# Performance work log

Measured on AMD Instinct MI355X. Metric: run time of the kernel, lower is better.

The kernel has to match this reference:

```python
import jax, jax.numpy as jnp
import numpy as np

TEMPERATURE = 0.04
LAMBDA_KOLEO = 0.1
EPS_NORM = 1e-12
EPS_KOLEO = 1e-9


def setup_inputs() -> dict:
    key = jax.random.key(0)
    k1, k2 = jax.random.split(key)
    N, D = 8192, 512
    z1 = jax.random.normal(k1, (N, D), dtype=jnp.float32)
    z2 = jax.random.normal(k2, (N, D), dtype=jnp.float32)
    return {"z1": z1, "z2": z2}


def _l2_normalize(x):
    # matches F.normalize(x, dim=1) with default eps=1e-12
    n = jnp.linalg.norm(x, axis=1, keepdims=True)
    return x / jnp.maximum(n, EPS_NORM)


def _infonce(queries, keys, temperature):
    # [N, N] similarity logits; labels are the diagonal
    logits = (queries @ keys.T) / temperature
    logp = jax.nn.log_softmax(logits, axis=1)
    return -jnp.mean(jnp.diagonal(logp))


def _koleo(emb):
    # pairwise euclidean distances via gram trick (matches torch.cdist p=2)
    sq = jnp.sum(emb * emb, axis=1)
    d2 = sq[:, None] + sq[None, :] - 2.0 * (emb @ emb.T)
    d = jnp.sqrt(jnp.maximum(d2, 0.0))
    N = emb.shape[0]
    eye = jnp.eye(N, dtype=bool)
    d = jnp.where(eye, jnp.inf, d)
    min_d = jnp.min(d, axis=1)
    return -jnp.mean(jnp.log(min_d + EPS_KOLEO))


def reference(z1, z2):
    z1 = _l2_normalize(z1)
    z2 = _l2_normalize(z2)
    loss_12 = _infonce(z1, z2, TEMPERATURE)
    loss_21 = _infonce(z2, z1, TEMPERATURE)
    loss_contrastive = (loss_12 + loss_21) / 2
    koleo_1 = _koleo(z1)
    koleo_2 = _koleo(z2)
    loss_koleo = (koleo_1 + koleo_2) / 2
    total_loss = loss_contrastive + LAMBDA_KOLEO * loss_koleo
    return total_loss
```

## Files before the change

kernel.cpp:

```cpp
#include <hip/hip_runtime.h>
#include <hip/hip_bf16.h>
#include <hip/hip_fp8.h>
#include <math.h>

#define N 8192
#define D 512
#define BM 128
#define BK 64
#define NSTRIP 64
#define S_BLOCKS (NSTRIP * NSTRIP)
#define TRI (NSTRIP * (NSTRIP + 1) / 2)
#define G_BLOCKS (2 * TRI)
#define SG_BLOCKS (S_BLOCKS + G_BLOCKS)

typedef float f32x16 __attribute__((ext_vector_type(16)));
typedef int i32x4 __attribute__((ext_vector_type(4)));
typedef int i32x8 __attribute__((ext_vector_type(8)));

__device__ inline void gload_lds16(const void* g, void* l) {
  __builtin_amdgcn_global_load_lds(
      (const __attribute__((address_space(1))) void*)g,
      (__attribute__((address_space(3))) void*)l, 16, 0, 0);
}

__global__ __launch_bounds__(256) void norm_kernel(
    const float* __restrict__ z1, const float* __restrict__ z2,
    unsigned char* __restrict__ q1, unsigned char* __restrict__ q2,
    float* __restrict__ diag, float* __restrict__ out) {
  int t = threadIdx.x;
  int lane = t & 63;
  int w = t >> 6;
  int row = blockIdx.x * 4 + w;
  if (blockIdx.x == 0 && t == 0) out[0] = 0.0f;
  const float4* a = (const float4*)(z1 + (size_t)row * D);
  const float4* b = (const float4*)(z2 + (size_t)row * D);
  float4 xa0 = a[lane], xa1 = a[lane + 64];
  float4 xb0 = b[lane], xb1 = b[lane + 64];
  float ss1 = xa0.x * xa0.x + xa0.y * xa0.y + xa0.z * xa0.z + xa0.w * xa0.w +
              xa1.x * xa1.x + xa1.y * xa1.y + xa1.z * xa1.z + xa1.w * xa1.w;
  float ss2 = xb0.x * xb0.x + xb0.y * xb0.y + xb0.z * xb0.z + xb0.w * xb0.w +
              xb1.x * xb1.x + xb1.y * xb1.y + xb1.z * xb1.z + xb1.w * xb1.w;
  float dd = xa0.x * xb0.x + xa0.y * xb0.y + xa0.z * xb0.z + xa0.w * xb0.w +
             xa1.x * xb1.x + xa1.y * xb1.y + xa1.z * xb1.z + xa1.w * xb1.w;
#pragma unroll
  for (int off = 1; off < 64; off <<= 1) {
    ss1 += __shfl_xor(ss1, off);
    ss2 += __shfl_xor(ss2, off);
    dd  += __shfl_xor(dd,  off);
  }
  float i1 = 1.0f / fmaxf(sqrtf(ss1), 1e-12f);
  float i2 = 1.0f / fmaxf(sqrtf(ss2), 1e-12f);
  float fa[8] = {xa0.x, xa0.y, xa0.z, xa0.w, xa1.x, xa1.y, xa1.z, xa1.w};
  float fb[8] = {xb0.x, xb0.y, xb0.z, xb0.w, xb1.x, xb1.y, xb1.z, xb1.w};
  unsigned int u1[2], u2[2];
#pragma unroll
  for (int g = 0; g < 2; g++) {
    unsigned int v1 = 0, v2 = 0;
#pragma unroll
    for (int e = 0; e < 4; e++) {
      __hip_fp8_e4m3 c1(fa[g * 4 + e] * i1);
      __hip_fp8_e4m3 c2(fb[g * 4 + e] * i2);
      v1 |= ((unsigned int)c1.__x) << (8 * e);
      v2 |= ((unsigned int)c2.__x) << (8 * e);
    }
    u1[g] = v1; u2[g] = v2;
  }
  ((unsigned int*)q1)[(size_t)row * 128 + lane] = u1[0];
  ((unsigned int*)q1)[(size_t)row * 128 + 64 + lane] = u1[1];
  ((unsigned int*)q2)[(size_t)row * 128 + lane] = u2[0];
  ((unsigned int*)q2)[(size_t)row * 128 + 64 + lane] = u2[1];
  if (lane == 0) diag[row] = dd * i1 * i2;
}

__device__ __forceinline__ void stage_chunk(
    const unsigned char* pA, const unsigned char* pB,
    unsigned char (*lds)[16384], int t, int chunk) {
  unsigned char* buf = lds[chunk & 1];
  int k0 = chunk * BK;
  gload_lds16(pA + k0,          buf + t * 16);
  gload_lds16(pA + 64 * D + k0, buf + 4096 + t * 16);
  gload_lds16(pB + k0,          buf + 8192 + t * 16);
  gload_lds16(pB + 64 * D + k0, buf + 12288 + t * 16);
}

#define SG_ROUND(p)                                                            \
  {                                                                            \
    asm volatile("s_waitcnt vmcnt(0)" ::: "memory");                           \
    __builtin_amdgcn_s_barrier();                                              \
    __builtin_amdgcn_sched_barrier(0);                                         \
    if ((p) < 7) stage_chunk(pA, pB, lds, t, (p) + 1);                         \
    const unsigned char* buf = lds[(p) & 1];                                   \
    i32x8 af[2], bf[2];                                                        \
    _Pragma("unroll")                                                          \
    for (int i = 0; i < 2; i++) {                                              \
      i32x4 lo = *(const i32x4*)(buf + offA[i]);                               \
      i32x4 hi = *(const i32x4*)(buf + (offA[i] ^ 16));                        \
      af[i] = __builtin_shufflevector(lo, hi, 0, 1, 2, 3, 4, 5, 6, 7);         \
      lo = *(const i32x4*)(buf + offB[i]);                                     \
      hi = *(const i32x4*)(buf + (offB[i] ^ 16));                              \
      bf[i] = __builtin_shufflevector(lo, hi, 0, 1, 2, 3, 4, 5, 6, 7);         \
    }                                                                          \
    asm volatile("s_waitcnt lgkmcnt(0)" ::: "memory");                         \
    __builtin_amdgcn_sched_barrier(0);                                         \
    __builtin_amdgcn_s_setprio(1);                                             \
    _Pragma("unroll")                                                          \
    for (int i = 0; i < 2; i++)                                                \
      _Pragma("unroll")                                                        \
      for (int j = 0; j < 2; j++)                                              \
        acc[i][j] = __builtin_amdgcn_mfma_scale_f32_32x32x64_f8f6f4(           \
            af[i], bf[j], acc[i][j], 0, 0, 0, 0x7F7F7F7F, 0, 0x7F7F7F7F);      \
    __builtin_amdgcn_s_setprio(0);                                             \
    __builtin_amdgcn_sched_barrier(0);                                         \
  }

__global__ __launch_bounds__(256, 4) void sg_kernel(
    const unsigned char* __restrict__ q1, const unsigned char* __restrict__ q2,
    float* __restrict__ rowS, float* __restrict__ colS,
    float* __restrict__ partG) {
  __shared__ unsigned char lds[2][16384];
  float (*redA)[BM] = reinterpret_cast<float (*)[BM]>(&lds[0][0]);
  float (*redB)[BM] = reinterpret_cast<float (*)[BM]>(&lds[0][0] + 1024);

  int bx = blockIdx.x;
  int t = threadIdx.x;
  int lane = t & 63;
  int wave = t >> 6;
  int l31 = lane & 31;
  int h = lane >> 5;
  int rw = wave >> 1;
  int cw = wave & 1;
  const float scale = 1.4426950408889634f / 0.04f;

  bool smode = bx < S_BLOCKS;
  const unsigned char* X;
  const unsigned char* Y;
  int r0, c0, ga = 0, gb = 0, gg = 0;
  bool diagb = false;
  if (smode) {
    r0 = (bx >> 6) * BM;
    c0 = (bx & 63) * BM;
    X = q1; Y = q2;
  } else {
    int gx = bx - S_BLOCKS;
    gg = (gx >= TRI) ? 1 : 0;
    int tri = gx - gg * TRI;
    int a = (int)((sqrtf(8.0f * (float)tri + 1.0f) - 1.0f) * 0.5f);
    while ((a + 1) * (a + 2) / 2 <= tri) a++;
    while (a * (a + 1) / 2 > tri) a--;
    int b = tri - a * (a + 1) / 2;
    ga = a; gb = b;
    X = gg ? q2 : q1; Y = X;
    r0 = a * BM;
    c0 = b * BM;
    diagb = (a == b);
  }

  int u = (l31 >> 4) & 1;
  int f = (l31 >> 1) & 3;
  int cs0 = (h << 1) ^ u ^ f;
  int offA[2], offB[2];
#pragma unroll
  for (int i = 0; i < 2; i++) {
    int rowa = rw * 64 + i * 32 + l31;
    offA[i] = rowa * 64 + cs0 * 16;
    int rowb = cw * 64 + i * 32 + l31;
    offB[i] = 8192 + rowb * 64 + cs0 * 16;
  }

  int srow = t >> 2;
  int ssrc = (t & 3) ^ ((t >> 3) & 3) ^ ((t >> 6) & 1);
  const unsigned char* pA = X + (size_t)(r0 + srow) * D + ssrc * 16;
  const unsigned char* pB = Y + (size_t)(c0 + srow) * D + ssrc * 16;

  f32x16 acc[2][2];
#pragma unroll
  for (int i = 0; i < 2; i++)
#pragma unroll
    for (int j = 0; j < 2; j++)
#pragma unroll
      for (int r = 0; r < 16; r++) acc[i][j][r] = 0.0f;

  stage_chunk(pA, pB, lds, t, 0);

  SG_ROUND(0) SG_ROUND(1) SG_ROUND(2) SG_ROUND(3)
  SG_ROUND(4) SG_ROUND(5) SG_ROUND(6) SG_ROUND(7)

  __syncthreads();

  if (smode) {
    float csum[2] = {0.0f, 0.0f};
#pragma unroll
    for (int i = 0; i < 2; i++) {
      float rsum[16];
#pragma unroll
      for (int reg = 0; reg < 16; reg++) rsum[reg] = 0.0f;
#pragma unroll
      for (int j = 0; j < 2; j++)
#pragma unroll
        for (int reg = 0; reg < 16; reg++) {
          float e = __builtin_amdgcn_exp2f(acc[i][j][reg] * scale);
          rsum[reg] += e;
          csum[j] += e;
        }
#pragma unroll
      for (int reg = 0; reg < 16; reg++) {
#pragma unroll
        for (int off = 1; off < 32; off <<= 1) rsum[reg] += __shfl_xor(rsum[reg], off);
      }
      if (l31 == 0) {
#pragma unroll
        for (int reg = 0; reg < 16; reg++) {
          int rloc = (reg & 3) + 8 * (reg >> 2) + 4 * h;
          redB[cw][rw * 64 + i * 32 + rloc] = rsum[reg];
        }
      }
    }
#pragma unroll
    for (int j = 0; j < 2; j++) {
      csum[j] += __shfl_xor(csum[j], 32);
      if (h == 0) redA[rw][cw * 64 + j * 32 + l31] = csum[j];
    }
    __syncthreads();
    if (t < BM) {
      colS[(size_t)(r0 >> 7) * N + c0 + t] = redA[0][t] + redA[1][t];
      rowS[(size_t)(c0 >> 7) * N + r0 + t] = redB[0][t] + redB[1][t];
    }
  } else {
#pragma unroll
    for (int i = 0; i < 2; i++) {
      float rmax[16];
#pragma unroll
      for (int reg = 0; reg < 16; reg++) {
        int rloc = (reg & 3) + 8 * (reg >> 2) + 4 * h;
        int rr = rw * 64 + i * 32 + rloc;
        float v = -3.0e38f;
#pragma unroll
        for (int j = 0; j < 2; j++) {
          float x = acc[i][j][reg];
          int cc = cw * 64 + j * 32 + l31;
          if (diagb && cc == rr) x = -3.0e38f;
          v = fmaxf(v, x);
        }
        rmax[reg] = v;
      }
#pragma unroll
      for (int reg = 0; reg < 16; reg++) {
#pragma unroll
        for (int off = 1; off < 32; off <<= 1) rmax[reg] = fmaxf(rmax[reg], __shfl_xor(rmax[reg], off));
      }
      if (l31 == 0) {
#pragma unroll
        for (int reg = 0; reg < 16; reg++) {
          int rloc = (reg & 3) + 8 * (reg >> 2) + 4 * h;
          redA[cw][rw * 64 + i * 32 + rloc] = rmax[reg];
        }
      }
    }
    if (!diagb) {
#pragma unroll
      for (int j = 0; j < 2; j++) {
        float m = -3.0e38f;
#pragma unroll
        for (int i = 0; i < 2; i++)
#pragma unroll
          for (int reg = 0; reg < 16; reg++) m = fmaxf(m, acc[i][j][reg]);
        m = fmaxf(m, __shfl_xor(m, 32));
        if (h == 0) redB[rw][cw * 64 + j * 32 + l31] = m;
      }
    }
    __syncthreads();
    if (t < BM) {
      partG[((size_t)(gg * NSTRIP + gb)) * N + r0 + t] = fmaxf(redA[0][t], redA[1][t]);
      if (!diagb)
        partG[((size_t)(gg * NSTRIP + ga)) * N + c0 + t] = fmaxf(redB[0][t], redB[1][t]);
    }
  }
}

__global__ __launch_bounds__(256) void combine_kernel(
    const float* __restrict__ diag,
    const float* __restrict__ rowS, const float* __restrict__ colS,
    const float* __restrict__ partG, float* __restrict__ out) {
  int t = threadIdx.x;
  int l = t & 63;
  int w = t >> 6;
  int i = blockIdx.x * 64 + l;

  float sR = 0.0f, sC = 0.0f, g1 = -3.0e38f, g2 = -3.0e38f;
#pragma unroll
  for (int s = 0; s < 16; s++) {
    int strip = w * 16 + s;
    sR += rowS[(size_t)strip * N + i];
    sC += colS[(size_t)strip * N + i];
    g1 = fmaxf(g1, partG[(size_t)strip * N + i]);
    g2 = fmaxf(g2, partG[(size_t)(NSTRIP + strip) * N + i]);
  }
  __shared__ float red[4][4][64];
  red[0][w][l] = sR; red[1][w][l] = sC; red[2][w][l] = g1; red[3][w][l] = g2;
  __syncthreads();
  if (w == 0) {
    sR = red[0][0][l] + red[0][1][l] + red[0][2][l] + red[0][3][l];
    sC = red[1][0][l] + red[1][1][l] + red[1][2][l] + red[1][3][l];
    g1 = fmaxf(fmaxf(red[2][0][l], red[2][1][l]), fmaxf(red[2][2][l], red[2][3][l]));
    g2 = fmaxf(fmaxf(red[3][0][l], red[3][1][l]), fmaxf(red[3][2][l], red[3][3][l]));
    float dv = diag[i] * 25.0f;
    float a12 = logf(sR) - dv;
    float a21 = logf(sC) - dv;
    float k1 = logf(sqrtf(fmaxf(2.0f - 2.0f * g1, 0.0f)) + 1e-9f);
    float k2 = logf(sqrtf(fmaxf(2.0f - 2.0f * g2, 0.0f)) + 1e-9f);
    float c = 0.5f * (a12 + a21) / (float)N - 0.1f * 0.5f * (k1 + k2) / (float)N;
#pragma unroll
    for (int off = 1; off < 64; off <<= 1) c += __shfl_xor(c, off);
    if (l == 0) atomicAdd(out, c);
  }
}

extern "C" void kernel_launch(void* const* d_in, const int* in_sizes, int n_in,
                              void* d_out, int out_size, void* d_ws, size_t ws_size,
                              hipStream_t stream) {
  const float* z1 = (const float*)d_in[0];
  const float* z2 = (const float*)d_in[1];
  char* w = (char*)d_ws;
  unsigned char* q1 = (unsigned char*)w; w += (size_t)N * D;
  unsigned char* q2 = (unsigned char*)w; w += (size_t)N * D;
  float* diag = (float*)w;   w += (size_t)N * sizeof(float);
  float* rowS = (float*)w;   w += (size_t)NSTRIP * N * sizeof(float);
  float* colS = (float*)w;   w += (size_t)NSTRIP * N * sizeof(float);
  float* partG = (float*)w;  w += (size_t)2 * NSTRIP * N * sizeof(float);
  float* out = (float*)d_out;

  norm_kernel<<<N / 4, 256, 0, stream>>>(z1, z2, q1, q2, diag, out);
  sg_kernel<<<SG_BLOCKS, 256, 0, stream>>>(q1, q2, rowS, colS, partG);
  combine_kernel<<<N / 64, 256, 0, stream>>>(diag, rowS, colS, partG, out);
}
```

Before: 199.9 us.

## Double K-chunk size to 128 with new LDS swizzle, halving barrier rounds

Raises the K staging chunk from 64 to 128 bytes, so each round loads a 128x128 fp8 tile of A and B into 32KB LDS buffers and issues two MFMA k-steps per round. The number of barrier and wait rounds drops from 8 to 4. LDS addressing changes to an XOR swizzle over 8 16-byte slots per 128-byte row. In exchange LDS use per block doubles and launch bounds drop from 4 to 2 blocks per CU, which lowers occupancy and the latency hiding it provides.

```diff
diff --git a/kernel.cpp b/kernel.cpp
--- a/kernel.cpp
+++ b/kernel.cpp
@@ -6,7 +6,7 @@
 #define N 8192
 #define D 512
 #define BM 128
-#define BK 64
+#define BK 128
 #define NSTRIP 64
 #define S_BLOCKS (NSTRIP * NSTRIP)
 #define TRI (NSTRIP * (NSTRIP + 1) / 2)
@@ -72,15 +72,15 @@
   if (lane == 0) diag[row] = dd * i1 * i2;
 }
 
-__device__ __forceinline__ void stage_chunk(
+__device__ __forceinline__ void stage_super(
     const unsigned char* pA, const unsigned char* pB,
-    unsigned char (*lds)[16384], int t, int chunk) {
-  unsigned char* buf = lds[chunk & 1];
-  int k0 = chunk * BK;
-  gload_lds16(pA + k0,          buf + t * 16);
-  gload_lds16(pA + 64 * D + k0, buf + 4096 + t * 16);
-  gload_lds16(pB + k0,          buf + 8192 + t * 16);
-  gload_lds16(pB + 64 * D + k0, buf + 12288 + t * 16);
+    unsigned char* buf, int t, int sc) {
+  int k0 = sc * BK;
+#pragma unroll
+  for (int it = 0; it < 4; it++) {
+    gload_lds16(pA + (size_t)(it * 32) * D + k0, buf + it * 4096 + t * 16);
+    gload_lds16(pB + (size_t)(it * 32) * D + k0, buf + 16384 + it * 4096 + t * 16);
+  }
 }
 
 #define SG_ROUND(p)                                                            \
@@ -88,36 +88,41 @@
     asm volatile("s_waitcnt vmcnt(0)" ::: "memory");                           \
     __builtin_amdgcn_s_barrier();                                              \
     __builtin_amdgcn_sched_barrier(0);                                         \
-    if ((p) < 7) stage_chunk(pA, pB, lds, t, (p) + 1);                         \
+    if ((p) < 3) stage_super(pA, pB, lds[((p) + 1) & 1], t, (p) + 1);          \
     const unsigned char* buf = lds[(p) & 1];                                   \
-    i32x8 af[2], bf[2];                                                        \
+    i32x8 af[2][2], bf[2][2];                                                  \
     _Pragma("unroll")                                                          \
-    for (int i = 0; i < 2; i++) {                                              \
-      i32x4 lo = *(const i32x4*)(buf + offA[i]);                               \
-      i32x4 hi = *(const i32x4*)(buf + (offA[i] ^ 16));                        \
-      af[i] = __builtin_shufflevector(lo, hi, 0, 1, 2, 3, 4, 5, 6, 7);         \
-      lo = *(const i32x4*)(buf + offB[i]);                                     \
-      hi = *(const i32x4*)(buf + (offB[i] ^ 16));                              \
-      bf[i] = __builtin_shufflevector(lo, hi, 0, 1, 2, 3, 4, 5, 6, 7);         \
-    }                                                                          \
+    for (int ks = 0; ks < 2; ks++)                                             \
+      _Pragma("unroll")                                                        \
+      for (int i = 0; i < 2; i++) {                                            \
+        i32x4 lo = *(const i32x4*)(buf + offA[ks][i]);                         \
+        i32x4 hi = *(const i32x4*)(buf + (offA[ks][i] ^ 16));                  \
+        af[ks][i] = __builtin_shufflevector(lo, hi, 0, 1, 2, 3, 4, 5, 6, 7);   \
+        lo = *(const i32x4*)(buf + offB[ks][i]);                               \
+        hi = *(const i32x4*)(buf + (offB[ks][i] ^ 16));                        \
+        bf[ks][i] = __builtin_shufflevector(lo, hi, 0, 1, 2, 3, 4, 5, 6, 7);   \
+      }                                                                        \
     asm volatile("s_waitcnt lgkmcnt(0)" ::: "memory");                         \
     __builtin_amdgcn_sched_barrier(0);                                         \
     __builtin_amdgcn_s_setprio(1);                                             \
     _Pragma("unroll")                                                          \
-    for (int i = 0; i < 2; i++)                                                \
+    for (int ks = 0; ks < 2; ks++)                                             \
       _Pragma("unroll")                                                        \
-      for (int j = 0; j < 2; j++)                                              \
-        acc[i][j] = __builtin_amdgcn_mfma_scale_f32_32x32x64_f8f6f4(           \
-            af[i], bf[j], acc[i][j], 0, 0, 0, 0x7F7F7F7F, 0, 0x7F7F7F7F);      \
+      for (int i = 0; i < 2; i++)                                              \
+        _Pragma("unroll")                                                      \
+        for (int j = 0; j < 2; j++)                                            \
+          acc[i][j] = __builtin_amdgcn_mfma_scale_f32_32x32x64_f8f6f4(         \
+              af[ks][i], bf[ks][j], acc[i][j], 0, 0, 0, 0x7F7F7F7F, 0,         \
+              0x7F7F7F7F);                                                     \
     __builtin_amdgcn_s_setprio(0);                                             \
     __builtin_amdgcn_sched_barrier(0);                                         \
   }
 
-__global__ __launch_bounds__(256, 4) void sg_kernel(
+__global__ __launch_bounds__(256, 2) void sg_kernel(
     const unsigned char* __restrict__ q1, const unsigned char* __restrict__ q2,
     float* __restrict__ rowS, float* __restrict__ colS,
     float* __restrict__ partG) {
-  __shared__ unsigned char lds[2][16384];
+  __shared__ unsigned char lds[2][32768];
   float (*redA)[BM] = reinterpret_cast<float (*)[BM]>(&lds[0][0]);
   float (*redB)[BM] = reinterpret_cast<float (*)[BM]>(&lds[0][0] + 1024);
 
@@ -155,20 +160,20 @@
     diagb = (a == b);
   }
 
-  int u = (l31 >> 4) & 1;
-  int f = (l31 >> 1) & 3;
-  int cs0 = (h << 1) ^ u ^ f;
-  int offA[2], offB[2];
-#pragma unroll
-  for (int i = 0; i < 2; i++) {
-    int rowa = rw * 64 + i * 32 + l31;
-    offA[i] = rowa * 64 + cs0 * 16;
-    int rowb = cw * 64 + i * 32 + l31;
-    offB[i] = 8192 + rowb * 64 + cs0 * 16;
-  }
-
-  int srow = t >> 2;
-  int ssrc = (t & 3) ^ ((t >> 3) & 3) ^ ((t >> 6) & 1);
+  int offA[2][2], offB[2][2];
+#pragma unroll
+  for (int ks = 0; ks < 2; ks++) {
+#pragma unroll
+    for (int i = 0; i < 2; i++) {
+      int rowa = rw * 64 + i * 32 + l31;
+      offA[ks][i] = rowa * 128 + (((ks << 2) | (h << 1)) ^ (rowa & 7)) * 16;
+      int rowb = cw * 64 + i * 32 + l31;
+      offB[ks][i] = 16384 + rowb * 128 + (((ks << 2) | (h << 1)) ^ (rowb & 7)) * 16;
+    }
+  }
+
+  int srow = t >> 3;
+  int ssrc = (t & 7) ^ ((t >> 3) & 7);
   const unsigned char* pA = X + (size_t)(r0 + srow) * D + ssrc * 16;
   const unsigned char* pB = Y + (size_t)(c0 + srow) * D + ssrc * 16;
 
@@ -180,10 +185,9 @@
 #pragma unroll
       for (int r = 0; r < 16; r++) acc[i][j][r] = 0.0f;
 
-  stage_chunk(pA, pB, lds, t, 0);
+  stage_super(pA, pB, lds[0], t, 0);
 
   SG_ROUND(0) SG_ROUND(1) SG_ROUND(2) SG_ROUND(3)
-  SG_ROUND(4) SG_ROUND(5) SG_ROUND(6) SG_ROUND(7)
 
   __syncthreads();
 
```

New measurement: 232.8 us. 1.16x slower.
